# Kernel optimization log

Measured on AMD Instinct MI355X. Metric: run time of the kernel, lower is better.

## Reference

```python
import jax, jax.numpy as jnp
import numpy as np

HID = 128


def setup_inputs() -> dict:
    key = jax.random.key(0)
    ks = jax.random.split(key, 7)
    B = 131072
    X = jax.random.normal(ks[0], (B, 4), dtype=jnp.float32)
    # Linear params stored as (in, out); scaled ~ 1/sqrt(fan_in) like torch default
    W1 = jax.random.normal(ks[1], (4, HID), dtype=jnp.float32) * 0.5
    b1 = jnp.zeros((HID,), jnp.float32)
    W2 = jax.random.normal(ks[2], (HID, HID), dtype=jnp.float32) * (1.0 / np.sqrt(HID))
    b2 = jnp.zeros((HID,), jnp.float32)
    W3 = jax.random.normal(ks[3], (HID, 1), dtype=jnp.float32) * (1.0 / np.sqrt(HID))
    b3 = jnp.zeros((1,), jnp.float32)
    return {"X": X, "W1": W1, "b1": b1, "W2": W2, "b2": b2, "W3": W3, "b3": b3}


def reference(X, W1, b1, W2, b2, W3, b3):
    def V_fn(feat):  # feat: [4] -> scalar potential
        h = jnp.tanh(feat @ W1 + b1)
        h = jnp.tanh(h @ W2 + b2)
        return (h @ W3 + b3)[0]

    def L_single(q, qd):  # q:[2], qd:[2] -> scalar Lagrangian
        t1, t2 = q[0], q[1]
        w1, w2 = qd[0], qd[1]
        T = w1 ** 2 + 0.5 * w2 ** 2 + w1 * w2 * jnp.cos(t1 - t2)
        feat = jnp.stack([jnp.sin(t1), jnp.cos(t1), jnp.sin(t2), jnp.cos(t2)])
        return T - V_fn(feat)

    q = X[:, :2]
    qd = X[:, 2:]
    dL_dq = jax.vmap(jax.grad(L_single, argnums=0))(q, qd)          # [B,2]
    # mass matrix M[i,j] = d^2 L / (d qd_i d qd_j)
    M = jax.vmap(jax.jacfwd(jax.grad(L_single, argnums=1), argnums=1))(q, qd)  # [B,2,2]
    # cross Hessian H[i,j] = d^2 L / (d qd_i d q_j); Coriolis C_i = H[i,:] @ qd
    H = jax.vmap(jax.jacfwd(jax.grad(L_single, argnums=1), argnums=0))(q, qd)  # [B,2,2]
    C = jnp.einsum('bij,bj->bi', H, qd)                              # [B,2]
    qdd = jnp.linalg.solve(M, (dL_dq - C)[..., None])[..., 0]        # [B,2]
    return jnp.concatenate([qd, qdd], axis=1)                        # [B,4]
```

## Files before the change

kernel.cpp:

```cpp
#include <hip/hip_runtime.h>
#include <math.h>

#define HID 128
#define SPB 64
#define TPB 512
#define GRIDB 512

typedef __bf16 bf16;
typedef bf16 bf16x8 __attribute__((ext_vector_type(8)));
typedef bf16 bf16x4 __attribute__((ext_vector_type(4)));
typedef float floatx4 __attribute__((ext_vector_type(4)));

__device__ __forceinline__ floatx4 tanh4(floatx4 z) {
    floatx4 t = z * 2.885390081777927f;
    floatx4 e = { __builtin_amdgcn_exp2f(t[0]), __builtin_amdgcn_exp2f(t[1]),
                  __builtin_amdgcn_exp2f(t[2]), __builtin_amdgcn_exp2f(t[3]) };
    e = e + 1.0f;
    floatx4 r = { __builtin_amdgcn_rcpf(e[0]), __builtin_amdgcn_rcpf(e[1]),
                  __builtin_amdgcn_rcpf(e[2]), __builtin_amdgcn_rcpf(e[3]) };
    return 1.0f - 2.0f * r;
}


__global__ __launch_bounds__(TPB, 4)
void lnn_kernel(const float* __restrict__ X,
                const float* __restrict__ W1,
                const float* __restrict__ b1,
                const float* __restrict__ b2,
                const float* __restrict__ W3,
                const float* __restrict__ W2,
                float* __restrict__ out,
                int B, int nchunk)
{
    __shared__ __align__(16) bf16 sBuf[16384];
    __shared__ __align__(16) float sW1r[4][HID];
    __shared__ __align__(16) float sB1[HID], sB2[HID], sW3[HID];
    __shared__ __align__(16) float sFeat[2][SPB][4];
    __shared__ float sQd[2][SPB][2];
    __shared__ __align__(16) float sDV[4][SPB][4];

    bf16* const sH1 = sBuf;
    bf16* const sG2 = sBuf + 8192;

    const int tid  = threadIdx.x;
    const int w    = tid >> 6;
    const int lane = tid & 63;
    const int lrow = lane & 15;
    const int lq   = lane >> 4;
    const int wlo  = w & 3;
    const int whi  = w >> 2;

    {
        int r = tid >> 7, j = tid & (HID - 1);
        sW1r[r][j] = W1[r * HID + j];
    }
    if (tid < HID) sB1[tid] = b1[tid];
    else if (tid < 2 * HID) sB2[tid - HID] = b2[tid - HID];
    else if (tid < 3 * HID) sW3[tid - 2 * HID] = W3[tid - 2 * HID];

    #pragma unroll
    for (int tt = 0; tt < 4; ++tt) {
        int e = tid + tt * TPB;
        int t = e >> 6, l = e & 63;
        int jt = t >> 2, kt = t & 3;
        int lr = l & 15, q = l >> 4;
        bf16x8 f;
        #pragma unroll
        for (int idx = 0; idx < 8; ++idx)
            f[idx] = (bf16)W2[(32*kt + 8*q + idx) * HID + 16*jt + lr];
        *reinterpret_cast<bf16x8*>(&sBuf[e * 8]) = f;
    }
    bf16x8 bW1 = {};
    if (lrow < 4) {
        const float4* wp = reinterpret_cast<const float4*>(&W1[lrow*HID + 32*wlo + 8*lq]);
        float4 a = wp[0], b = wp[1];
        bW1[0]=(bf16)a.x; bW1[1]=(bf16)a.y; bW1[2]=(bf16)a.z; bW1[3]=(bf16)a.w;
        bW1[4]=(bf16)b.x; bW1[5]=(bf16)b.y; bW1[6]=(bf16)b.z; bW1[7]=(bf16)b.w;
    }
    bf16x8 aW2[2][4];
    #pragma unroll
    for (int u = 0; u < 2; ++u) {
        const float* rbase = &W2[(16*(2*wlo + u) + lrow) * HID + 8*lq];
        #pragma unroll
        for (int jt2 = 0; jt2 < 4; ++jt2) {
            const float4* rp = reinterpret_cast<const float4*>(rbase + 32*jt2);
            float4 r0 = rp[0], r1 = rp[1];
            bf16x8 g;
            g[0]=(bf16)r0.x; g[1]=(bf16)r0.y; g[2]=(bf16)r0.z; g[3]=(bf16)r0.w;
            g[4]=(bf16)r1.x; g[5]=(bf16)r1.y; g[6]=(bf16)r1.z; g[7]=(bf16)r1.w;
            aW2[u][jt2] = g;
        }
    }
    if (tid >= TPB - SPB) {
        int s  = tid - (TPB - SPB);
        int g  = (int)blockIdx.x * SPB + s;
        int gc = g < B ? g : (B - 1);
        float4 x = reinterpret_cast<const float4*>(X)[gc];
        float s1, c1, s2, c2;
        __sincosf(x.x, &s1, &c1);
        __sincosf(x.y, &s2, &c2);
        sFeat[0][s][0]=s1; sFeat[0][s][1]=c1; sFeat[0][s][2]=s2; sFeat[0][s][3]=c2;
        sQd[0][s][0]=x.z;  sQd[0][s][1]=x.w;
    }
    __syncthreads();

    bf16x8 aW2T[2][4];
    #pragma unroll
    for (int u = 0; u < 2; ++u)
        #pragma unroll
        for (int kt = 0; kt < 4; ++kt)
            aW2T[u][kt] = *reinterpret_cast<const bf16x8*>(&sBuf[(((2*wlo+u)*4 + kt)*64 + lane)*8]);
    __syncthreads();

    #pragma unroll 1
    for (int c = 0; c < nchunk; ++c) {
        const int par = c & 1;
        const int s0  = (c * GRIDB + (int)blockIdx.x) * SPB;

        {
            int s = 16 * wlo + lrow;
            float f0 = sFeat[par][s][0], f1 = sFeat[par][s][1];
            float f2 = sFeat[par][s][2], f3 = sFeat[par][s][3];
            #pragma unroll
            for (int h = 0; h < 2; ++h) {
                int kt = 2 * whi + h;
                int jb = 32 * kt + 8 * lq;
                floatx4 w0a = *reinterpret_cast<const floatx4*>(&sW1r[0][jb]);
                floatx4 w0b = *reinterpret_cast<const floatx4*>(&sW1r[0][jb+4]);
                floatx4 w1a = *reinterpret_cast<const floatx4*>(&sW1r[1][jb]);
                floatx4 w1b = *reinterpret_cast<const floatx4*>(&sW1r[1][jb+4]);
                floatx4 w2a = *reinterpret_cast<const floatx4*>(&sW1r[2][jb]);
                floatx4 w2b = *reinterpret_cast<const floatx4*>(&sW1r[2][jb+4]);
                floatx4 w3a = *reinterpret_cast<const floatx4*>(&sW1r[3][jb]);
                floatx4 w3b = *reinterpret_cast<const floatx4*>(&sW1r[3][jb+4]);
                floatx4 bba = *reinterpret_cast<const floatx4*>(&sB1[jb]);
                floatx4 bbb = *reinterpret_cast<const floatx4*>(&sB1[jb+4]);
                floatx4 za = bba + f0*w0a + f1*w1a + f2*w2a + f3*w3a;
                floatx4 zb = bbb + f0*w0b + f1*w1b + f2*w2b + f3*w3b;
                floatx4 ha = tanh4(za);
                floatx4 hb = tanh4(zb);
                bf16x8 hf;
                hf[0]=(bf16)ha[0]; hf[1]=(bf16)ha[1]; hf[2]=(bf16)ha[2]; hf[3]=(bf16)ha[3];
                hf[4]=(bf16)hb[0]; hf[5]=(bf16)hb[1]; hf[6]=(bf16)hb[2]; hf[7]=(bf16)hb[3];
                *reinterpret_cast<bf16x8*>(&sH1[((wlo*4 + kt)*64 + lane)*8]) = hf;
            }
        }
        __syncthreads();

        floatx4 acc[2][2];
        #pragma unroll
        for (int t = 0; t < 2; ++t)
            #pragma unroll
            for (int s = 0; s < 2; ++s) acc[t][s] = floatx4{0.f,0.f,0.f,0.f};
        #pragma unroll
        for (int kt = 0; kt < 4; ++kt) {
            bf16x8 b0 = *reinterpret_cast<const bf16x8*>(&sH1[(((2*whi  )*4 + kt)*64 + lane)*8]);
            bf16x8 b1v = *reinterpret_cast<const bf16x8*>(&sH1[(((2*whi+1)*4 + kt)*64 + lane)*8]);
            acc[0][0] = __builtin_amdgcn_mfma_f32_16x16x32_bf16(aW2T[0][kt], b0,  acc[0][0], 0,0,0);
            acc[0][1] = __builtin_amdgcn_mfma_f32_16x16x32_bf16(aW2T[0][kt], b1v, acc[0][1], 0,0,0);
            acc[1][0] = __builtin_amdgcn_mfma_f32_16x16x32_bf16(aW2T[1][kt], b0,  acc[1][0], 0,0,0);
            acc[1][1] = __builtin_amdgcn_mfma_f32_16x16x32_bf16(aW2T[1][kt], b1v, acc[1][1], 0,0,0);
        }

        #pragma unroll
        for (int t = 0; t < 2; ++t) {
            int jb = 16*(2*wlo + t) + 4*lq;
            floatx4 b2v = *reinterpret_cast<const floatx4*>(&sB2[jb]);
            floatx4 w3v = *reinterpret_cast<const floatx4*>(&sW3[jb]);
            int q2  = 2*t + (lq >> 1);
            int sub = 4 * (lq & 1);
            #pragma unroll
            for (int s = 0; s < 2; ++s) {
                int st = 2*whi + s;
                floatx4 h = tanh4(acc[t][s] + b2v);
                floatx4 gv = (1.0f - h*h) * w3v;
                bf16x4 g;
                g[0]=(bf16)gv[0]; g[1]=(bf16)gv[1]; g[2]=(bf16)gv[2]; g[3]=(bf16)gv[3];
                *reinterpret_cast<bf16x4*>(&sG2[((st*4 + wlo)*64 + (q2*16 + lrow))*8 + sub]) = g;
            }
        }
        __syncthreads();

        #pragma unroll
        for (int t = 0; t < 2; ++t)
            #pragma unroll
            for (int s = 0; s < 2; ++s) acc[t][s] = floatx4{0.f,0.f,0.f,0.f};
        #pragma unroll
        for (int jt2 = 0; jt2 < 4; ++jt2) {
            bf16x8 g0 = *reinterpret_cast<const bf16x8*>(&sG2[(((2*whi  )*4 + jt2)*64 + lane)*8]);
            bf16x8 g1 = *reinterpret_cast<const bf16x8*>(&sG2[(((2*whi+1)*4 + jt2)*64 + lane)*8]);
            acc[0][0] = __builtin_amdgcn_mfma_f32_16x16x32_bf16(aW2[0][jt2], g0, acc[0][0], 0,0,0);
            acc[0][1] = __builtin_amdgcn_mfma_f32_16x16x32_bf16(aW2[0][jt2], g1, acc[0][1], 0,0,0);
            acc[1][0] = __builtin_amdgcn_mfma_f32_16x16x32_bf16(aW2[1][jt2], g0, acc[1][0], 0,0,0);
            acc[1][1] = __builtin_amdgcn_mfma_f32_16x16x32_bf16(aW2[1][jt2], g1, acc[1][1], 0,0,0);
        }

        #pragma unroll
        for (int u = 0; u < 2; ++u) {
            int q2  = 2*u + (lq >> 1);
            int sub = 4 * (lq & 1);
            #pragma unroll
            for (int s = 0; s < 2; ++s) {
                int st  = 2*whi + s;
                int off = ((st*4 + wlo)*64 + (q2*16 + lrow))*8 + sub;
                bf16x4 h4 = *reinterpret_cast<const bf16x4*>(&sH1[off]);
                floatx4 hf = { (float)h4[0], (float)h4[1], (float)h4[2], (float)h4[3] };
                floatx4 gv = (1.0f - hf*hf) * acc[u][s];
                bf16x4 g;
                g[0]=(bf16)gv[0]; g[1]=(bf16)gv[1]; g[2]=(bf16)gv[2]; g[3]=(bf16)gv[3];
                *reinterpret_cast<bf16x4*>(&sH1[off]) = g;
            }
        }

        if (tid >= TPB - SPB && c + 1 < nchunk) {
            int s  = tid - (TPB - SPB);
            int g  = ((c + 1) * GRIDB + (int)blockIdx.x) * SPB + s;
            int gc = g < B ? g : (B - 1);
            float4 x = reinterpret_cast<const float4*>(X)[gc];
            float s1, c1, s2, c2;
            __sincosf(x.x, &s1, &c1);
            __sincosf(x.y, &s2, &c2);
            int np = par ^ 1;
            sFeat[np][s][0]=s1; sFeat[np][s][1]=c1; sFeat[np][s][2]=s2; sFeat[np][s][3]=c2;
            sQd[np][s][0]=x.z;  sQd[np][s][1]=x.w;
        }

        {
            bf16x8 g0 = *reinterpret_cast<const bf16x8*>(&sH1[(((2*whi  )*4 + wlo)*64 + lane)*8]);
            bf16x8 g1 = *reinterpret_cast<const bf16x8*>(&sH1[(((2*whi+1)*4 + wlo)*64 + lane)*8]);
            floatx4 d0 = __builtin_amdgcn_mfma_f32_16x16x32_bf16(bW1, g0, floatx4{0.f,0.f,0.f,0.f}, 0,0,0);
            floatx4 d1 = __builtin_amdgcn_mfma_f32_16x16x32_bf16(bW1, g1, floatx4{0.f,0.f,0.f,0.f}, 0,0,0);
            if (lane < 16) {
                *reinterpret_cast<float4*>(&sDV[wlo][16*(2*whi  ) + lane][0]) =
                    make_float4(d0[0], d0[1], d0[2], d0[3]);
                *reinterpret_cast<float4*>(&sDV[wlo][16*(2*whi+1) + lane][0]) =
                    make_float4(d1[0], d1[1], d1[2], d1[3]);
            }
        }
        __syncthreads();

        if (tid < SPB) {
            int g = s0 + tid;
            if (g < B) {
                floatx4 d0 = *reinterpret_cast<const floatx4*>(&sDV[0][tid][0]);
                floatx4 d1 = *reinterpret_cast<const floatx4*>(&sDV[1][tid][0]);
                floatx4 d2 = *reinterpret_cast<const floatx4*>(&sDV[2][tid][0]);
                floatx4 d3 = *reinterpret_cast<const floatx4*>(&sDV[3][tid][0]);
                floatx4 dV = (d0 + d1) + (d2 + d3);
                float s1 = sFeat[par][tid][0], c1 = sFeat[par][tid][1];
                float s2 = sFeat[par][tid][2], c2 = sFeat[par][tid][3];
                float w1 = sQd[par][tid][0],  w2 = sQd[par][tid][1];
                float cosD = c1 * c2 + s1 * s2;
                float sinD = s1 * c2 - c1 * s2;
                float dVt1 = dV[0] * c1 - dV[1] * s1;
                float dVt2 = dV[2] * c2 - dV[3] * s2;
                float sT = w1 * w2 * sinD;
                float cw = sinD * (w2 - w1);
                float rhs1 = (-sT - dVt1) - w2 * cw;
                float rhs2 = ( sT - dVt2) - w1 * cw;
                float det = 2.0f - cosD * cosD;
                float inv = __builtin_amdgcn_rcpf(det);
                float qdd1 = (rhs1 - cosD * rhs2) * inv;
                float qdd2 = (2.0f * rhs2 - cosD * rhs1) * inv;
                *reinterpret_cast<float4*>(&out[4 * g]) = make_float4(w1, w2, qdd1, qdd2);
            }
        }
    }
}

extern "C" void kernel_launch(void* const* d_in, const int* in_sizes, int n_in,
                              void* d_out, int out_size, void* d_ws, size_t ws_size,
                              hipStream_t stream) {
    const float* X  = (const float*)d_in[0];
    const float* W1 = (const float*)d_in[1];
    const float* b1 = (const float*)d_in[2];
    const float* W2 = (const float*)d_in[3];
    const float* b2 = (const float*)d_in[4];
    const float* W3 = (const float*)d_in[5];
    float* out = (float*)d_out;
    int B = in_sizes[0] / 4;
    int nchunk = (B + GRIDB * SPB - 1) / (GRIDB * SPB);
    lnn_kernel<<<GRIDB, TPB, 0, stream>>>(X, W1, b1, b2, W3, W2, out, B, nchunk);
}
```

Baseline: 91.03 us.

## Give each wavefront its own 16-sample tile to remove block-wide barriers

Restructures the kernel so each of 16 wavefronts independently processes a 16-sample tile end to end. It stores both W2 layouts in shared memory and keeps per-wave scratch for hidden activations and gradients, which removes all __syncthreads from the main loop. It also prefetches the next tile's inputs into registers. The trade-off is that every wave now streams W2 fragments from LDS for each MFMA instead of holding them in registers, raising LDS traffic. The larger shared-memory footprint and 1024-thread blocks also change occupancy.

```diff
diff --git a/kernel.cpp b/kernel.cpp
--- a/kernel.cpp
+++ b/kernel.cpp
@@ -2,9 +2,9 @@
 #include <math.h>
 
 #define HID 128
-#define SPB 64
-#define TPB 512
-#define GRIDB 512
+#define TPB 1024
+#define NW  16
+#define GRIDB 256
 
 typedef __bf16 bf16;
 typedef bf16 bf16x8 __attribute__((ext_vector_type(8)));
@@ -32,239 +32,181 @@
                 float* __restrict__ out,
                 int B, int nchunk)
 {
-    __shared__ __align__(16) bf16 sBuf[16384];
+    __shared__ __align__(16) bf16 sW2A[16384];
+    __shared__ __align__(16) bf16 sW2R[16384];
+    __shared__ __align__(16) bf16 sH1w[NW][2048];
+    __shared__ __align__(16) bf16 sGl[NW][512];
     __shared__ __align__(16) float sW1r[4][HID];
     __shared__ __align__(16) float sB1[HID], sB2[HID], sW3[HID];
-    __shared__ __align__(16) float sFeat[2][SPB][4];
-    __shared__ float sQd[2][SPB][2];
-    __shared__ __align__(16) float sDV[4][SPB][4];
-
-    bf16* const sH1 = sBuf;
-    bf16* const sG2 = sBuf + 8192;
 
     const int tid  = threadIdx.x;
     const int w    = tid >> 6;
     const int lane = tid & 63;
     const int lrow = lane & 15;
     const int lq   = lane >> 4;
-    const int wlo  = w & 3;
-    const int whi  = w >> 2;
-
-    {
-        int r = tid >> 7, j = tid & (HID - 1);
-        sW1r[r][j] = W1[r * HID + j];
-    }
+
+    if (tid < 512) { int r = tid >> 7, j = tid & (HID - 1); sW1r[r][j] = W1[r * HID + j]; }
     if (tid < HID) sB1[tid] = b1[tid];
     else if (tid < 2 * HID) sB2[tid - HID] = b2[tid - HID];
     else if (tid < 3 * HID) sW3[tid - 2 * HID] = W3[tid - 2 * HID];
 
     #pragma unroll
-    for (int tt = 0; tt < 4; ++tt) {
+    for (int tt = 0; tt < 2; ++tt) {
         int e = tid + tt * TPB;
         int t = e >> 6, l = e & 63;
-        int jt = t >> 2, kt = t & 3;
+        int a = t >> 2, bidx = t & 3;
         int lr = l & 15, q = l >> 4;
         bf16x8 f;
         #pragma unroll
         for (int idx = 0; idx < 8; ++idx)
-            f[idx] = (bf16)W2[(32*kt + 8*q + idx) * HID + 16*jt + lr];
-        *reinterpret_cast<bf16x8*>(&sBuf[e * 8]) = f;
+            f[idx] = (bf16)W2[(32*bidx + 8*q + idx) * HID + 16*a + lr];
+        *reinterpret_cast<bf16x8*>(&sW2A[e * 8]) = f;
+        const float4* rp = reinterpret_cast<const float4*>(&W2[(16*a + lr) * HID + 32*bidx + 8*q]);
+        float4 r0 = rp[0], r1 = rp[1];
+        bf16x8 g;
+        g[0]=(bf16)r0.x; g[1]=(bf16)r0.y; g[2]=(bf16)r0.z; g[3]=(bf16)r0.w;
+        g[4]=(bf16)r1.x; g[5]=(bf16)r1.y; g[6]=(bf16)r1.z; g[7]=(bf16)r1.w;
+        *reinterpret_cast<bf16x8*>(&sW2R[e * 8]) = g;
     }
-    bf16x8 bW1 = {};
+    bf16x8 bW1[4];
+    #pragma unroll
+    for (int m = 0; m < 4; ++m) { bf16x8 z = {}; bW1[m] = z; }
     if (lrow < 4) {
-        const float4* wp = reinterpret_cast<const float4*>(&W1[lrow*HID + 32*wlo + 8*lq]);
-        float4 a = wp[0], b = wp[1];
-        bW1[0]=(bf16)a.x; bW1[1]=(bf16)a.y; bW1[2]=(bf16)a.z; bW1[3]=(bf16)a.w;
-        bW1[4]=(bf16)b.x; bW1[5]=(bf16)b.y; bW1[6]=(bf16)b.z; bW1[7]=(bf16)b.w;
-    }
-    bf16x8 aW2[2][4];
-    #pragma unroll
-    for (int u = 0; u < 2; ++u) {
-        const float* rbase = &W2[(16*(2*wlo + u) + lrow) * HID + 8*lq];
-        #pragma unroll
-        for (int jt2 = 0; jt2 < 4; ++jt2) {
-            const float4* rp = reinterpret_cast<const float4*>(rbase + 32*jt2);
-            float4 r0 = rp[0], r1 = rp[1];
-            bf16x8 g;
-            g[0]=(bf16)r0.x; g[1]=(bf16)r0.y; g[2]=(bf16)r0.z; g[3]=(bf16)r0.w;
-            g[4]=(bf16)r1.x; g[5]=(bf16)r1.y; g[6]=(bf16)r1.z; g[7]=(bf16)r1.w;
-            aW2[u][jt2] = g;
-        }
-    }
-    if (tid >= TPB - SPB) {
-        int s  = tid - (TPB - SPB);
-        int g  = (int)blockIdx.x * SPB + s;
-        int gc = g < B ? g : (B - 1);
-        float4 x = reinterpret_cast<const float4*>(X)[gc];
-        float s1, c1, s2, c2;
-        __sincosf(x.x, &s1, &c1);
-        __sincosf(x.y, &s2, &c2);
-        sFeat[0][s][0]=s1; sFeat[0][s][1]=c1; sFeat[0][s][2]=s2; sFeat[0][s][3]=c2;
-        sQd[0][s][0]=x.z;  sQd[0][s][1]=x.w;
+        #pragma unroll
+        for (int m = 0; m < 4; ++m) {
+            const float4* wp = reinterpret_cast<const float4*>(&W1[lrow*HID + 32*m + 8*lq]);
+            float4 a = wp[0], b = wp[1];
+            bW1[m][0]=(bf16)a.x; bW1[m][1]=(bf16)a.y; bW1[m][2]=(bf16)a.z; bW1[m][3]=(bf16)a.w;
+            bW1[m][4]=(bf16)b.x; bW1[m][5]=(bf16)b.y; bW1[m][6]=(bf16)b.z; bW1[m][7]=(bf16)b.w;
+        }
     }
     __syncthreads();
 
-    bf16x8 aW2T[2][4];
-    #pragma unroll
-    for (int u = 0; u < 2; ++u)
-        #pragma unroll
-        for (int kt = 0; kt < 4; ++kt)
-            aW2T[u][kt] = *reinterpret_cast<const bf16x8*>(&sBuf[(((2*wlo+u)*4 + kt)*64 + lane)*8]);
-    __syncthreads();
+    bf16* const myH = &sH1w[w][0];
+    bf16* const myG = &sGl[w][0];
+
+    const int tileStride = GRIDB * NW;
+    const int t0 = (int)blockIdx.x * NW + w;
+    int gc0 = t0 * 16 + lrow; gc0 = gc0 < B ? gc0 : (B - 1);
+    float4 xc = reinterpret_cast<const float4*>(X)[gc0];
 
     #pragma unroll 1
     for (int c = 0; c < nchunk; ++c) {
-        const int par = c & 1;
-        const int s0  = (c * GRIDB + (int)blockIdx.x) * SPB;
-
+        const int tile = t0 + c * tileStride;
+        if (tile * 16 >= B) break;
+        const int S0 = tile * 16;
+
+        float s1, c1, s2, c2;
+        __sincosf(xc.x, &s1, &c1);
+        __sincosf(xc.y, &s2, &c2);
+        const float qd1 = xc.z, qd2 = xc.w;
+
+        float4 xn = xc;
         {
-            int s = 16 * wlo + lrow;
-            float f0 = sFeat[par][s][0], f1 = sFeat[par][s][1];
-            float f2 = sFeat[par][s][2], f3 = sFeat[par][s][3];
+            int tn = tile + tileStride;
+            if (tn * 16 < B) {
+                int gc = tn * 16 + lrow; gc = gc < B ? gc : (B - 1);
+                xn = reinterpret_cast<const float4*>(X)[gc];
+            }
+        }
+
+        bf16x8 breg[4];
+        #pragma unroll
+        for (int kt = 0; kt < 4; ++kt) {
+            int jb = 32 * kt + 8 * lq;
+            floatx4 w0a = *reinterpret_cast<const floatx4*>(&sW1r[0][jb]);
+            floatx4 w0b = *reinterpret_cast<const floatx4*>(&sW1r[0][jb+4]);
+            floatx4 w1a = *reinterpret_cast<const floatx4*>(&sW1r[1][jb]);
+            floatx4 w1b = *reinterpret_cast<const floatx4*>(&sW1r[1][jb+4]);
+            floatx4 w2a = *reinterpret_cast<const floatx4*>(&sW1r[2][jb]);
+            floatx4 w2b = *reinterpret_cast<const floatx4*>(&sW1r[2][jb+4]);
+            floatx4 w3a = *reinterpret_cast<const floatx4*>(&sW1r[3][jb]);
+            floatx4 w3b = *reinterpret_cast<const floatx4*>(&sW1r[3][jb+4]);
+            floatx4 bba = *reinterpret_cast<const floatx4*>(&sB1[jb]);
+            floatx4 bbb = *reinterpret_cast<const floatx4*>(&sB1[jb+4]);
+            floatx4 za = bba + s1*w0a + c1*w1a + s2*w2a + c2*w3a;
+            floatx4 zb = bbb + s1*w0b + c1*w1b + s2*w2b + c2*w3b;
+            floatx4 ha = tanh4(za);
+            floatx4 hb = tanh4(zb);
+            bf16x8 hf;
+            hf[0]=(bf16)ha[0]; hf[1]=(bf16)ha[1]; hf[2]=(bf16)ha[2]; hf[3]=(bf16)ha[3];
+            hf[4]=(bf16)hb[0]; hf[5]=(bf16)hb[1]; hf[6]=(bf16)hb[2]; hf[7]=(bf16)hb[3];
+            breg[kt] = hf;
+            *reinterpret_cast<bf16x8*>(&myH[(kt*64 + lane)*8]) = hf;
+        }
+
+        floatx4 acc[8];
+        #pragma unroll
+        for (int jt = 0; jt < 8; ++jt) acc[jt] = floatx4{0.f,0.f,0.f,0.f};
+        #pragma unroll
+        for (int jt = 0; jt < 8; ++jt)
             #pragma unroll
-            for (int h = 0; h < 2; ++h) {
-                int kt = 2 * whi + h;
-                int jb = 32 * kt + 8 * lq;
-                floatx4 w0a = *reinterpret_cast<const floatx4*>(&sW1r[0][jb]);
-                floatx4 w0b = *reinterpret_cast<const floatx4*>(&sW1r[0][jb+4]);
-                floatx4 w1a = *reinterpret_cast<const floatx4*>(&sW1r[1][jb]);
-                floatx4 w1b = *reinterpret_cast<const floatx4*>(&sW1r[1][jb+4]);
-                floatx4 w2a = *reinterpret_cast<const floatx4*>(&sW1r[2][jb]);
-                floatx4 w2b = *reinterpret_cast<const floatx4*>(&sW1r[2][jb+4]);
-                floatx4 w3a = *reinterpret_cast<const floatx4*>(&sW1r[3][jb]);
-                floatx4 w3b = *reinterpret_cast<const floatx4*>(&sW1r[3][jb+4]);
-                floatx4 bba = *reinterpret_cast<const floatx4*>(&sB1[jb]);
-                floatx4 bbb = *reinterpret_cast<const floatx4*>(&sB1[jb+4]);
-                floatx4 za = bba + f0*w0a + f1*w1a + f2*w2a + f3*w3a;
-                floatx4 zb = bbb + f0*w0b + f1*w1b + f2*w2b + f3*w3b;
-                floatx4 ha = tanh4(za);
-                floatx4 hb = tanh4(zb);
-                bf16x8 hf;
-                hf[0]=(bf16)ha[0]; hf[1]=(bf16)ha[1]; hf[2]=(bf16)ha[2]; hf[3]=(bf16)ha[3];
-                hf[4]=(bf16)hb[0]; hf[5]=(bf16)hb[1]; hf[6]=(bf16)hb[2]; hf[7]=(bf16)hb[3];
-                *reinterpret_cast<bf16x8*>(&sH1[((wlo*4 + kt)*64 + lane)*8]) = hf;
-            }
-        }
-        __syncthreads();
-
-        floatx4 acc[2][2];
-        #pragma unroll
-        for (int t = 0; t < 2; ++t)
+            for (int kt = 0; kt < 4; ++kt)
+                acc[jt] = __builtin_amdgcn_mfma_f32_16x16x32_bf16(
+                    *reinterpret_cast<const bf16x8*>(&sW2A[((jt*4 + kt)*64 + lane)*8]),
+                    breg[kt], acc[jt], 0,0,0);
+
+        floatx4 acc2[8];
+        #pragma unroll
+        for (int it = 0; it < 8; ++it) acc2[it] = floatx4{0.f,0.f,0.f,0.f};
+        #pragma unroll
+        for (int jt2 = 0; jt2 < 4; ++jt2) {
             #pragma unroll
-            for (int s = 0; s < 2; ++s) acc[t][s] = floatx4{0.f,0.f,0.f,0.f};
-        #pragma unroll
-        for (int kt = 0; kt < 4; ++kt) {
-            bf16x8 b0 = *reinterpret_cast<const bf16x8*>(&sH1[(((2*whi  )*4 + kt)*64 + lane)*8]);
-            bf16x8 b1v = *reinterpret_cast<const bf16x8*>(&sH1[(((2*whi+1)*4 + kt)*64 + lane)*8]);
-            acc[0][0] = __builtin_amdgcn_mfma_f32_16x16x32_bf16(aW2T[0][kt], b0,  acc[0][0], 0,0,0);
-            acc[0][1] = __builtin_amdgcn_mfma_f32_16x16x32_bf16(aW2T[0][kt], b1v, acc[0][1], 0,0,0);
-            acc[1][0] = __builtin_amdgcn_mfma_f32_16x16x32_bf16(aW2T[1][kt], b0,  acc[1][0], 0,0,0);
-            acc[1][1] = __builtin_amdgcn_mfma_f32_16x16x32_bf16(aW2T[1][kt], b1v, acc[1][1], 0,0,0);
-        }
-
-        #pragma unroll
-        for (int t = 0; t < 2; ++t) {
-            int jb = 16*(2*wlo + t) + 4*lq;
-            floatx4 b2v = *reinterpret_cast<const floatx4*>(&sB2[jb]);
-            floatx4 w3v = *reinterpret_cast<const floatx4*>(&sW3[jb]);
-            int q2  = 2*t + (lq >> 1);
-            int sub = 4 * (lq & 1);
-            #pragma unroll
-            for (int s = 0; s < 2; ++s) {
-                int st = 2*whi + s;
-                floatx4 h = tanh4(acc[t][s] + b2v);
+            for (int b = 0; b < 2; ++b) {
+                int jt = 2*jt2 + b;
+                int jb = 16*jt + 4*lq;
+                floatx4 b2v = *reinterpret_cast<const floatx4*>(&sB2[jb]);
+                floatx4 w3v = *reinterpret_cast<const floatx4*>(&sW3[jb]);
+                floatx4 h = tanh4(acc[jt] + b2v);
                 floatx4 gv = (1.0f - h*h) * w3v;
                 bf16x4 g;
                 g[0]=(bf16)gv[0]; g[1]=(bf16)gv[1]; g[2]=(bf16)gv[2]; g[3]=(bf16)gv[3];
-                *reinterpret_cast<bf16x4*>(&sG2[((st*4 + wlo)*64 + (q2*16 + lrow))*8 + sub]) = g;
+                *reinterpret_cast<bf16x4*>(&myG[((2*b + (lq>>1))*16 + lrow)*8 + 4*(lq&1)]) = g;
             }
-        }
-        __syncthreads();
-
-        #pragma unroll
-        for (int t = 0; t < 2; ++t)
+            bf16x8 gB = *reinterpret_cast<const bf16x8*>(&myG[lane*8]);
             #pragma unroll
-            for (int s = 0; s < 2; ++s) acc[t][s] = floatx4{0.f,0.f,0.f,0.f};
-        #pragma unroll
-        for (int jt2 = 0; jt2 < 4; ++jt2) {
-            bf16x8 g0 = *reinterpret_cast<const bf16x8*>(&sG2[(((2*whi  )*4 + jt2)*64 + lane)*8]);
-            bf16x8 g1 = *reinterpret_cast<const bf16x8*>(&sG2[(((2*whi+1)*4 + jt2)*64 + lane)*8]);
-            acc[0][0] = __builtin_amdgcn_mfma_f32_16x16x32_bf16(aW2[0][jt2], g0, acc[0][0], 0,0,0);
-            acc[0][1] = __builtin_amdgcn_mfma_f32_16x16x32_bf16(aW2[0][jt2], g1, acc[0][1], 0,0,0);
-            acc[1][0] = __builtin_amdgcn_mfma_f32_16x16x32_bf16(aW2[1][jt2], g0, acc[1][0], 0,0,0);
-            acc[1][1] = __builtin_amdgcn_mfma_f32_16x16x32_bf16(aW2[1][jt2], g1, acc[1][1], 0,0,0);
-        }
-
-        #pragma unroll
-        for (int u = 0; u < 2; ++u) {
-            int q2  = 2*u + (lq >> 1);
-            int sub = 4 * (lq & 1);
-            #pragma unroll
-            for (int s = 0; s < 2; ++s) {
-                int st  = 2*whi + s;
-                int off = ((st*4 + wlo)*64 + (q2*16 + lrow))*8 + sub;
-                bf16x4 h4 = *reinterpret_cast<const bf16x4*>(&sH1[off]);
-                floatx4 hf = { (float)h4[0], (float)h4[1], (float)h4[2], (float)h4[3] };
-                floatx4 gv = (1.0f - hf*hf) * acc[u][s];
-                bf16x4 g;
-                g[0]=(bf16)gv[0]; g[1]=(bf16)gv[1]; g[2]=(bf16)gv[2]; g[3]=(bf16)gv[3];
-                *reinterpret_cast<bf16x4*>(&sH1[off]) = g;
-            }
-        }
-
-        if (tid >= TPB - SPB && c + 1 < nchunk) {
-            int s  = tid - (TPB - SPB);
-            int g  = ((c + 1) * GRIDB + (int)blockIdx.x) * SPB + s;
-            int gc = g < B ? g : (B - 1);
-            float4 x = reinterpret_cast<const float4*>(X)[gc];
-            float s1, c1, s2, c2;
-            __sincosf(x.x, &s1, &c1);
-            __sincosf(x.y, &s2, &c2);
-            int np = par ^ 1;
-            sFeat[np][s][0]=s1; sFeat[np][s][1]=c1; sFeat[np][s][2]=s2; sFeat[np][s][3]=c2;
-            sQd[np][s][0]=x.z;  sQd[np][s][1]=x.w;
-        }
-
-        {
-            bf16x8 g0 = *reinterpret_cast<const bf16x8*>(&sH1[(((2*whi  )*4 + wlo)*64 + lane)*8]);
-            bf16x8 g1 = *reinterpret_cast<const bf16x8*>(&sH1[(((2*whi+1)*4 + wlo)*64 + lane)*8]);
-            floatx4 d0 = __builtin_amdgcn_mfma_f32_16x16x32_bf16(bW1, g0, floatx4{0.f,0.f,0.f,0.f}, 0,0,0);
-            floatx4 d1 = __builtin_amdgcn_mfma_f32_16x16x32_bf16(bW1, g1, floatx4{0.f,0.f,0.f,0.f}, 0,0,0);
-            if (lane < 16) {
-                *reinterpret_cast<float4*>(&sDV[wlo][16*(2*whi  ) + lane][0]) =
-                    make_float4(d0[0], d0[1], d0[2], d0[3]);
-                *reinterpret_cast<float4*>(&sDV[wlo][16*(2*whi+1) + lane][0]) =
-                    make_float4(d1[0], d1[1], d1[2], d1[3]);
-            }
-        }
-        __syncthreads();
-
-        if (tid < SPB) {
-            int g = s0 + tid;
-            if (g < B) {
-                floatx4 d0 = *reinterpret_cast<const floatx4*>(&sDV[0][tid][0]);
-                floatx4 d1 = *reinterpret_cast<const floatx4*>(&sDV[1][tid][0]);
-                floatx4 d2 = *reinterpret_cast<const floatx4*>(&sDV[2][tid][0]);
-                floatx4 d3 = *reinterpret_cast<const floatx4*>(&sDV[3][tid][0]);
-                floatx4 dV = (d0 + d1) + (d2 + d3);
-                float s1 = sFeat[par][tid][0], c1 = sFeat[par][tid][1];
-                float s2 = sFeat[par][tid][2], c2 = sFeat[par][tid][3];
-                float w1 = sQd[par][tid][0],  w2 = sQd[par][tid][1];
-                float cosD = c1 * c2 + s1 * s2;
-                float sinD = s1 * c2 - c1 * s2;
-                float dVt1 = dV[0] * c1 - dV[1] * s1;
-                float dVt2 = dV[2] * c2 - dV[3] * s2;
-                float sT = w1 * w2 * sinD;
-                float cw = sinD * (w2 - w1);
-                float rhs1 = (-sT - dVt1) - w2 * cw;
-                float rhs2 = ( sT - dVt2) - w1 * cw;
-                float det = 2.0f - cosD * cosD;
-                float inv = __builtin_amdgcn_rcpf(det);
-                float qdd1 = (rhs1 - cosD * rhs2) * inv;
-                float qdd2 = (2.0f * rhs2 - cosD * rhs1) * inv;
-                *reinterpret_cast<float4*>(&out[4 * g]) = make_float4(w1, w2, qdd1, qdd2);
-            }
-        }
+            for (int it = 0; it < 8; ++it)
+                acc2[it] = __builtin_amdgcn_mfma_f32_16x16x32_bf16(
+                    *reinterpret_cast<const bf16x8*>(&sW2R[((it*4 + jt2)*64 + lane)*8]),
+                    gB, acc2[it], 0,0,0);
+        }
+
+        #pragma unroll
+        for (int it = 0; it < 8; ++it) {
+            int off = ((it>>1)*64 + ((2*(it&1) + (lq>>1))*16 + lrow))*8 + 4*(lq&1);
+            bf16x4 h4 = *reinterpret_cast<const bf16x4*>(&myH[off]);
+            floatx4 hf = { (float)h4[0], (float)h4[1], (float)h4[2], (float)h4[3] };
+            floatx4 gv = (1.0f - hf*hf) * acc2[it];
+            bf16x4 g;
+            g[0]=(bf16)gv[0]; g[1]=(bf16)gv[1]; g[2]=(bf16)gv[2]; g[3]=(bf16)gv[3];
+            *reinterpret_cast<bf16x4*>(&myH[off]) = g;
+        }
+
+        floatx4 dv = floatx4{0.f,0.f,0.f,0.f};
+        #pragma unroll
+        for (int m = 0; m < 4; ++m)
+            dv = __builtin_amdgcn_mfma_f32_16x16x32_bf16(
+                bW1[m],
+                *reinterpret_cast<const bf16x8*>(&myH[(m*64 + lane)*8]),
+                dv, 0,0,0);
+
+        if (lane < 16 && S0 + lane < B) {
+            float dV0 = dv[0], dV1 = dv[1], dV2 = dv[2], dV3 = dv[3];
+            float cosD = c1 * c2 + s1 * s2;
+            float sinD = s1 * c2 - c1 * s2;
+            float dVt1 = dV0 * c1 - dV1 * s1;
+            float dVt2 = dV2 * c2 - dV3 * s2;
+            float sT = qd1 * qd2 * sinD;
+            float cw = sinD * (qd2 - qd1);
+            float rhs1 = (-sT - dVt1) - qd2 * cw;
+            float rhs2 = ( sT - dVt2) - qd1 * cw;
+            float det = 2.0f - cosD * cosD;
+            float inv = __builtin_amdgcn_rcpf(det);
+            float qdd1 = (rhs1 - cosD * rhs2) * inv;
+            float qdd2 = (2.0f * rhs2 - cosD * rhs1) * inv;
+            *reinterpret_cast<float4*>(&out[4 * (S0 + lane)]) = make_float4(qd1, qd2, qdd1, qdd2);
+        }
+        xc = xn;
     }
 }
 
@@ -279,6 +221,7 @@
     const float* W3 = (const float*)d_in[5];
     float* out = (float*)d_out;
     int B = in_sizes[0] / 4;
-    int nchunk = (B + GRIDB * SPB - 1) / (GRIDB * SPB);
+    int tiles = (B + 15) >> 4;
+    int nchunk = (tiles + GRIDB * NW - 1) / (GRIDB * NW);
     lnn_kernel<<<GRIDB, TPB, 0, stream>>>(X, W1, b1, b2, W3, W2, out, B, nchunk);
 }
```

Result: faster. 88.61 us (-2.7%).
